# Kernel tuning notes

Measured on AMD Instinct MI355X. Metric: run time of the kernel, lower is better.

The kernel has to match this reference:

```python
import jax, jax.numpy as jnp
import numpy as np

B, N, ENC = 128, 196, 2048
DEC, ATT, EMB, V, T = 512, 512, 512, 10000, 21


def setup_inputs() -> dict:
    key = jax.random.key(0)
    ks = jax.random.split(key, 20)
    g = lambda k, shape, scale=0.02: jax.random.normal(k, shape, dtype=jnp.float32) * scale
    return {
        "features": jax.random.normal(ks[0], (B, N, ENC), dtype=jnp.float32),
        "captions": jax.random.randint(ks[1], (B, T), 0, V),
        "emb": g(ks[2], (V, EMB)),
        # attention (weights stored [in, out])
        "U_w": g(ks[3], (ENC, ATT)), "U_b": jnp.zeros((ATT,), jnp.float32),
        "W_w": g(ks[4], (DEC, ATT)), "W_b": jnp.zeros((ATT,), jnp.float32),
        "A_w": g(ks[5], (ATT, 1)),   "A_b": jnp.zeros((1,), jnp.float32),
        # init hidden state
        "ih_w": g(ks[6], (ENC, DEC)), "ih_b": jnp.zeros((DEC,), jnp.float32),
        "ic_w": g(ks[7], (ENC, DEC)), "ic_b": jnp.zeros((DEC,), jnp.float32),
        # LSTMCell, torch gate order (i, f, g, o); stored [in, 4*DEC]
        "lstm_Wih": g(ks[8], (EMB + ENC, 4 * DEC)),
        "lstm_Whh": g(ks[9], (DEC, 4 * DEC)),
        "lstm_bih": jnp.zeros((4 * DEC,), jnp.float32),
        "lstm_bhh": jnp.zeros((4 * DEC,), jnp.float32),
        # output projection
        "fcn_w": g(ks[10], (DEC, V)), "fcn_b": jnp.zeros((V,), jnp.float32),
    }


def reference(features, captions, emb, U_w, U_b, W_w, W_b, A_w, A_b,
              ih_w, ih_b, ic_w, ic_b,
              lstm_Wih, lstm_Whh, lstm_bih, lstm_bhh, fcn_w, fcn_b):
    # init hidden state from mean-pooled features
    mean_feat = features.mean(axis=1)                      # [B, ENC]
    h0 = mean_feat @ ih_w + ih_b                           # [B, DEC]
    c0 = mean_feat @ ic_w + ic_b

    # U(features) is constant across timesteps -> precompute
    u_hs = jnp.einsum('bne,ea->bna', features, U_w) + U_b  # [B, N, ATT]

    embeds = emb[captions[:, :T - 1]]                       # [B, S, EMB]
    embeds_t = jnp.swapaxes(embeds, 0, 1)                   # [S, B, EMB]

    def step(carry, emb_t):
        h, c = carry
        # Bahdanau attention
        w_ah = h @ W_w + W_b                                # [B, ATT]
        scores = (jnp.tanh(u_hs + w_ah[:, None, :]) @ A_w)[..., 0] + A_b[0]  # [B, N]
        alpha = jax.nn.softmax(scores, axis=1)
        context = jnp.einsum('bn,bne->be', alpha, features) # [B, ENC]
        # LSTMCell
        x = jnp.concatenate([emb_t, context], axis=1)       # [B, EMB+ENC]
        gates = x @ lstm_Wih + lstm_bih + h @ lstm_Whh + lstm_bhh
        i, f, g, o = jnp.split(gates, 4, axis=1)
        c = jax.nn.sigmoid(f) * c + jax.nn.sigmoid(i) * jnp.tanh(g)
        h = jax.nn.sigmoid(o) * jnp.tanh(c)
        out = h @ fcn_w + fcn_b                             # [B, V] (dropout = identity in eval)
        return (h, c), (out, alpha)

    (_, _), (preds_t, alphas_t) = jax.lax.scan(step, (h0, c0), embeds_t)
    preds = jnp.swapaxes(preds_t, 0, 1)                     # [B, S, V]
    alphas = jnp.swapaxes(alphas_t, 0, 1)                   # [B, S, N]
    return preds, alphas
```

## Files before the change

kernel.cpp:

```cpp
#include <hip/hip_runtime.h>
#include <cmath>

#define B_   128
#define N_   196
#define ENC_ 2048
#define DEC_ 512
#define ATT_ 512
#define EMB_ 512
#define V_   10000
#define TS_  20
#define HCAT_ 12672
#define HOUT_ 2560

typedef unsigned short u16;
typedef short s16x8 __attribute__((ext_vector_type(8)));
typedef float f32x4 __attribute__((ext_vector_type(4)));
typedef unsigned short u16x4 __attribute__((ext_vector_type(4)));

__device__ __forceinline__ float sigmoidf_(float x) { return 1.0f / (1.0f + expf(-x)); }

__device__ __forceinline__ u16 f2bf(float x) {
  union { float f; unsigned u; } v; v.f = x;
  unsigned r = v.u + 0x7fff + ((v.u >> 16) & 1);
  return (u16)(r >> 16);
}
__device__ __forceinline__ float bf2f(u16 h) {
  union { float f; unsigned u; } v; v.u = ((unsigned)h) << 16; return v.f;
}

typedef const __attribute__((address_space(1))) void gas_t;
typedef __attribute__((address_space(3))) void las_t;
__device__ __forceinline__ void gld_lds16(const void* g, void* l) {
  __builtin_amdgcn_global_load_lds((gas_t*)g, (las_t*)l, 16, 0, 0);
}

__global__ __launch_bounds__(256, 2) void k_mfma(
    const u16* __restrict__ A, int lda,
    const u16* __restrict__ Bt, int ldb,
    const float* __restrict__ bias,
    float* __restrict__ C, u16* __restrict__ Cb, int ldc, int Nbound,
    float* __restrict__ C2, int csplit, int ldc2,
    int K, int atomic) {
  __shared__ __align__(16) u16 As[128 * 32];
  __shared__ __align__(16) u16 Bs[128 * 32];

  const int tid = threadIdx.x;
  const int bm = blockIdx.y * 128;
  const int bn = blockIdx.x * 128;
  const int kchunk = K / gridDim.z;
  const int k0 = blockIdx.z * kchunk;
  const int kend = k0 + kchunk;

  const int r0 = tid >> 2;
  const int kb = (tid & 3) * 8;
  const u16* ga0 = A + (size_t)(bm + r0) * lda + kb;
  const u16* ga1 = A + (size_t)(bm + 64 + r0) * lda + kb;
  const u16* gb0 = Bt + (size_t)(bn + r0) * ldb + kb;
  const u16* gb1 = Bt + (size_t)(bn + 64 + r0) * ldb + kb;
  u16* la0 = As + tid * 8;
  u16* la1 = As + 2048 + tid * 8;
  u16* lb0 = Bs + tid * 8;
  u16* lb1 = Bs + 2048 + tid * 8;

  const int w = tid >> 6;
  const int lane = tid & 63;
  const int wm = (w & 1) * 64;
  const int wn = (w >> 1) * 64;
  const int r16 = lane & 15;
  const int kq = lane >> 4;

  f32x4 acc[4][4] = {};

  for (int k = k0; k < kend; k += 32) {
    gld_lds16(ga0 + k, la0);
    gld_lds16(ga1 + k, la1);
    gld_lds16(gb0 + k, lb0);
    gld_lds16(gb1 + k, lb1);
    __syncthreads();
    s16x8 af[4], bfr[4];
#pragma unroll
    for (int i = 0; i < 4; ++i)
      af[i] = *(const s16x8*)&As[(wm + i * 16 + r16) * 32 + kq * 8];
#pragma unroll
    for (int i = 0; i < 4; ++i)
      bfr[i] = *(const s16x8*)&Bs[(wn + i * 16 + r16) * 32 + kq * 8];
#pragma unroll
    for (int mi = 0; mi < 4; ++mi)
#pragma unroll
      for (int ni = 0; ni < 4; ++ni)
        acc[mi][ni] = __builtin_amdgcn_mfma_f32_16x16x32_bf16(af[mi], bfr[ni], acc[mi][ni], 0, 0, 0);
    __syncthreads();
  }

#pragma unroll
  for (int ni = 0; ni < 4; ++ni) {
    int col = bn + wn + ni * 16 + r16;
    if (col < Nbound) {
      float bv = bias ? bias[col] : 0.f;
#pragma unroll
      for (int mi = 0; mi < 4; ++mi) {
#pragma unroll
        for (int r = 0; r < 4; ++r) {
          int row = bm + wm + mi * 16 + kq * 4 + r;
          float v = acc[mi][ni][r] + bv;
          if (atomic)                     atomicAdd(&C[(size_t)row * ldc + col], v);
          else if (Cb)                    Cb[(size_t)row * ldc + col] = f2bf(v);
          else if (C2 && col >= csplit)   C2[(size_t)row * ldc2 + (col - csplit)] = v;
          else                            C[(size_t)row * ldc + col] = v;
        }
      }
    }
  }
}

__global__ __launch_bounds__(256) void k_wt(const float* __restrict__ in, int K, int N,
                                            u16* __restrict__ out, int ldo, int Nout) {
  __shared__ float s[32][33];
  int k0 = blockIdx.x * 32, n0 = blockIdx.y * 32;
  int tx = threadIdx.x & 31, ty = threadIdx.x >> 5;
#pragma unroll
  for (int i = 0; i < 4; ++i) {
    int k = k0 + ty + i * 8, n = n0 + tx;
    s[ty + i * 8][tx] = (n < N) ? in[(size_t)k * N + n] : 0.f;
  }
  __syncthreads();
#pragma unroll
  for (int i = 0; i < 4; ++i) {
    int n = n0 + ty + i * 8;
    if (n < Nout) out[(size_t)n * ldo + k0 + tx] = f2bf(s[tx][ty + i * 8]);
  }
}

__global__ __launch_bounds__(256) void k_hbias(const float* __restrict__ W_b,
                                               const float* __restrict__ bih,
                                               const float* __restrict__ bhh,
                                               const float* __restrict__ fcn_b,
                                               float* __restrict__ hbias) {
  int i = blockIdx.x * 256 + threadIdx.x;
  if (i >= HCAT_) return;
  float v;
  if (i < 512)        v = W_b[i];
  else if (i < 2560)  v = bih[i - 512] + bhh[i - 512];
  else if (i < 12560) v = fcn_b[i - 2560];
  else                v = 0.f;
  hbias[i] = v;
}

__global__ __launch_bounds__(256) void k_embed_all(const float* __restrict__ emb,
                                                   const int* __restrict__ captions,
                                                   u16* __restrict__ emb_all_bf) {
  int r = blockIdx.y;
  int t = r >> 7, b = r & 127;
  int k = blockIdx.x * 256 + threadIdx.x;
  int tok = captions[b * 21 + t];
  emb_all_bf[(size_t)r * EMB_ + k] = f2bf(emb[(size_t)tok * EMB_ + k]);
}

__global__ __launch_bounds__(256) void k_cvtmean(const float* __restrict__ f,
                                                 u16* __restrict__ feat_bf,
                                                 u16* __restrict__ mean_bf) {
  int b = blockIdx.y;
  int e = blockIdx.x * 256 + threadIdx.x;
  const float* p = f + (size_t)b * N_ * ENC_ + e;
  u16* q = feat_bf + (size_t)b * N_ * ENC_ + e;
  float s = 0.f;
#pragma unroll 4
  for (int n = 0; n < N_; ++n) {
    float v = p[(size_t)n * ENC_];
    s += v;
    q[(size_t)n * ENC_] = f2bf(v);
  }
  mean_bf[b * ENC_ + e] = f2bf(s * (1.0f / (float)N_));
}

__global__ __launch_bounds__(256) void k_scores(const u16* __restrict__ u_hs,
                                                const float* __restrict__ w_ah, int ldw,
                                                const float* __restrict__ A_w,
                                                const float* __restrict__ A_b,
                                                float* __restrict__ scores) {
  int wave = threadIdx.x >> 6;
  int lane = threadIdx.x & 63;
  int bn = blockIdx.x * 4 + wave;
  int b = bn / N_;
  int a0 = lane * 8;
  const u16* up = u_hs + (size_t)bn * ATT_ + a0;
  const float* wp = w_ah + (size_t)b * ldw + a0;
  float s = 0.f;
#pragma unroll
  for (int j = 0; j < 2; ++j) {
    u16x4 uv = *(const u16x4*)(up + j * 4);
    float4 wv = *(const float4*)(wp + j * 4);
    float4 aw = *(const float4*)(A_w + a0 + j * 4);
    s += tanhf(bf2f(uv.x) + wv.x) * aw.x;
    s += tanhf(bf2f(uv.y) + wv.y) * aw.y;
    s += tanhf(bf2f(uv.z) + wv.z) * aw.z;
    s += tanhf(bf2f(uv.w) + wv.w) * aw.w;
  }
#pragma unroll
  for (int off = 32; off; off >>= 1) s += __shfl_down(s, off);
  if (lane == 0) scores[bn] = s + A_b[0];
}

__global__ __launch_bounds__(256) void k_ctx(const float* __restrict__ scores,
                                             const u16* __restrict__ feat_bf,
                                             const float* __restrict__ embg_t,
                                             const float* __restrict__ houtt,
                                             float* __restrict__ gates,
                                             float* __restrict__ alphas, int t,
                                             u16* __restrict__ ctx_bf) {
  int b = blockIdx.y, tid = threadIdx.x;
  int w = tid >> 6, lane = tid & 63;

  {
    int j0 = blockIdx.x * 1024 + tid * 4;
    float4 eg = *(const float4*)(embg_t + (size_t)b * 2048 + j0);
    float4 hg = *(const float4*)(houtt + (size_t)b * HOUT_ + 512 + j0);
    float4 o; o.x = eg.x + hg.x; o.y = eg.y + hg.y; o.z = eg.z + hg.z; o.w = eg.w + hg.w;
    *(float4*)(gates + (size_t)b * 2048 + j0) = o;
  }

  __shared__ float al[N_];
  __shared__ float wm[4], ws[4];
  __shared__ float bmax, bsum;
  float v = (tid < N_) ? scores[b * N_ + tid] : -1e30f;
  float m = v;
#pragma unroll
  for (int off = 32; off; off >>= 1) m = fmaxf(m, __shfl_down(m, off));
  if (lane == 0) wm[w] = m;
  __syncthreads();
  if (tid == 0) bmax = fmaxf(fmaxf(wm[0], wm[1]), fmaxf(wm[2], wm[3]));
  __syncthreads();
  float e = (tid < N_) ? expf(v - bmax) : 0.f;
  float s = e;
#pragma unroll
  for (int off = 32; off; off >>= 1) s += __shfl_down(s, off);
  if (lane == 0) ws[w] = s;
  __syncthreads();
  if (tid == 0) bsum = ws[0] + ws[1] + ws[2] + ws[3];
  __syncthreads();
  float a = e / bsum;
  if (tid < N_) {
    al[tid] = a;
    if (blockIdx.x == 0) alphas[((size_t)b * TS_ + t) * N_ + tid] = a;
  }
  __syncthreads();

  int e0 = blockIdx.x * 1024 + tid * 4;
  const u16* fp = feat_bf + (size_t)b * N_ * ENC_ + e0;
  float s0 = 0, s1 = 0, s2 = 0, s3 = 0;
#pragma unroll 4
  for (int n = 0; n < N_; ++n) {
    u16x4 vv = *(const u16x4*)(fp + (size_t)n * ENC_);
    float av = al[n];
    s0 += av * bf2f(vv.x); s1 += av * bf2f(vv.y);
    s2 += av * bf2f(vv.z); s3 += av * bf2f(vv.w);
  }
  u16x4 o; o.x = f2bf(s0); o.y = f2bf(s1); o.z = f2bf(s2); o.w = f2bf(s3);
  *(u16x4*)(ctx_bf + (size_t)b * ENC_ + e0) = o;
}

__global__ __launch_bounds__(256) void k_lstm(const float* __restrict__ gates,
                                              float* __restrict__ c,
                                              u16* __restrict__ h_bf) {
  int b = blockIdx.y;
  int j = blockIdx.x * 256 + threadIdx.x;
  const float* g = gates + (size_t)b * 2048;
  float ig = sigmoidf_(g[j]);
  float fg = sigmoidf_(g[512 + j]);
  float gg = tanhf(g[1024 + j]);
  float og = sigmoidf_(g[1536 + j]);
  float cn = fg * c[b * DEC_ + j] + ig * gg;
  c[b * DEC_ + j] = cn;
  h_bf[(size_t)b * DEC_ + j] = f2bf(og * tanhf(cn));
}

extern "C" void kernel_launch(void* const* d_in, const int* in_sizes, int n_in,
                              void* d_out, int out_size, void* d_ws, size_t ws_size,
                              hipStream_t stream) {
  (void)in_sizes; (void)n_in; (void)out_size; (void)ws_size;

  const float* features = (const float*)d_in[0];
  const int*   captions = (const int*)d_in[1];
  const float* emb      = (const float*)d_in[2];
  const float* U_w      = (const float*)d_in[3];
  const float* U_b      = (const float*)d_in[4];
  const float* W_w      = (const float*)d_in[5];
  const float* W_b      = (const float*)d_in[6];
  const float* A_w      = (const float*)d_in[7];
  const float* A_b      = (const float*)d_in[8];
  const float* ih_w     = (const float*)d_in[9];
  const float* ih_b     = (const float*)d_in[10];
  const float* ic_w     = (const float*)d_in[11];
  const float* ic_b     = (const float*)d_in[12];
  const float* Wih      = (const float*)d_in[13];
  const float* Whh      = (const float*)d_in[14];
  const float* bih      = (const float*)d_in[15];
  const float* bhh      = (const float*)d_in[16];
  const float* fcn_w    = (const float*)d_in[17];
  const float* fcn_b    = (const float*)d_in[18];

  float* preds  = (float*)d_out;
  float* alphas = (float*)d_out + (size_t)B_ * TS_ * V_;

  float* p = (float*)d_ws;
  u16*   u_hs      = (u16*)p;    p += (size_t)B_ * N_ * ATT_ / 2;
  u16*   feat_bf   = (u16*)p;    p += (size_t)B_ * N_ * ENC_ / 2;
  u16*   hcatT     = (u16*)p;    p += (size_t)HCAT_ * DEC_ / 2;
  u16*   U_wT      = (u16*)p;    p += (size_t)ATT_ * ENC_ / 2;
  u16*   ih_wT     = (u16*)p;    p += (size_t)DEC_ * ENC_ / 2;
  u16*   ic_wT     = (u16*)p;    p += (size_t)DEC_ * ENC_ / 2;
  u16*   WihEmbT   = (u16*)p;    p += (size_t)2048 * EMB_ / 2;
  u16*   WihCtxT   = (u16*)p;    p += (size_t)2048 * ENC_ / 2;
  u16*   mean_bf   = (u16*)p;    p += (size_t)B_ * ENC_ / 2;
  u16*   emb_all   = (u16*)p;    p += (size_t)TS_ * B_ * EMB_ / 2;
  u16*   h_bf      = (u16*)p;    p += (size_t)B_ * DEC_ / 2;
  u16*   ctx_bf    = (u16*)p;    p += (size_t)B_ * ENC_ / 2;
  float* embgates  = p;          p += (size_t)TS_ * B_ * 2048;
  float* houtt     = p;          p += (size_t)B_ * HOUT_;
  float* cbuf      = p;          p += (size_t)B_ * DEC_;
  float* scores    = p;          p += (size_t)B_ * N_;
  float* gates     = p;          p += (size_t)B_ * 2048;
  float* hbias     = p;          p += HCAT_;

  k_cvtmean<<<dim3(ENC_ / 256, B_), 256, 0, stream>>>(features, feat_bf, mean_bf);
  k_wt<<<dim3(ENC_ / 32, ATT_ / 32), 256, 0, stream>>>(U_w, ENC_, ATT_, U_wT, ENC_, ATT_);
  k_wt<<<dim3(ENC_ / 32, DEC_ / 32), 256, 0, stream>>>(ih_w, ENC_, DEC_, ih_wT, ENC_, DEC_);
  k_wt<<<dim3(ENC_ / 32, DEC_ / 32), 256, 0, stream>>>(ic_w, ENC_, DEC_, ic_wT, ENC_, DEC_);
  k_wt<<<dim3(DEC_ / 32, ATT_ / 32), 256, 0, stream>>>(W_w, DEC_, ATT_, hcatT, DEC_, ATT_);
  k_wt<<<dim3(DEC_ / 32, 2048 / 32), 256, 0, stream>>>(Whh, DEC_, 2048, hcatT + (size_t)512 * DEC_, DEC_, 2048);
  k_wt<<<dim3(DEC_ / 32, 10112 / 32), 256, 0, stream>>>(fcn_w, DEC_, V_, hcatT + (size_t)2560 * DEC_, DEC_, 10112);
  k_wt<<<dim3(EMB_ / 32, 2048 / 32), 256, 0, stream>>>(Wih, EMB_, 2048, WihEmbT, EMB_, 2048);
  k_wt<<<dim3(ENC_ / 32, 2048 / 32), 256, 0, stream>>>(Wih + (size_t)EMB_ * 2048, ENC_, 2048, WihCtxT, ENC_, 2048);
  k_hbias<<<(HCAT_ + 255) / 256, 256, 0, stream>>>(W_b, bih, bhh, fcn_b, hbias);
  k_embed_all<<<dim3(EMB_ / 256, TS_ * B_), 256, 0, stream>>>(emb, captions, emb_all);

  k_mfma<<<dim3(4, 1, 1), 256, 0, stream>>>(mean_bf, ENC_, ih_wT, ENC_, ih_b,
                                            nullptr, h_bf, DEC_, DEC_, nullptr, 0, 0, ENC_, 0);
  k_mfma<<<dim3(4, 1, 1), 256, 0, stream>>>(mean_bf, ENC_, ic_wT, ENC_, ic_b,
                                            cbuf, nullptr, DEC_, DEC_, nullptr, 0, 0, ENC_, 0);
  k_mfma<<<dim3(ATT_ / 128, (B_ * N_) / 128, 1), 256, 0, stream>>>(
      feat_bf, ENC_, U_wT, ENC_, U_b, nullptr, u_hs, ATT_, ATT_, nullptr, 0, 0, ENC_, 0);
  k_mfma<<<dim3(2048 / 128, TS_, 1), 256, 0, stream>>>(
      emb_all, EMB_, WihEmbT, EMB_, nullptr, embgates, nullptr, 2048, 2048, nullptr, 0, 0, EMB_, 0);

  for (int t = 0; t < TS_; ++t) {
    if (t == 0) {
      k_mfma<<<dim3(HOUT_ / 128, 1, 1), 256, 0, stream>>>(
          h_bf, DEC_, hcatT, DEC_, hbias, houtt, nullptr, HOUT_, HOUT_,
          nullptr, 0, 0, DEC_, 0);
    } else {
      k_mfma<<<dim3(HCAT_ / 128, 1, 1), 256, 0, stream>>>(
          h_bf, DEC_, hcatT, DEC_, hbias, houtt, nullptr, HOUT_, 12560,
          preds + (size_t)(t - 1) * V_, HOUT_, TS_ * V_, DEC_, 0);
    }

    k_scores<<<(B_ * N_) / 4, 256, 0, stream>>>(u_hs, houtt, HOUT_, A_w, A_b, scores);

    k_ctx<<<dim3(2, B_), 256, 0, stream>>>(scores, feat_bf, embgates + (size_t)t * B_ * 2048,
                                           houtt, gates, alphas, t, ctx_bf);

    k_mfma<<<dim3(2048 / 128, 1, 8), 256, 0, stream>>>(
        ctx_bf, ENC_, WihCtxT, ENC_, nullptr, gates, nullptr, 2048, 2048, nullptr, 0, 0, ENC_, 1);

    k_lstm<<<dim3(DEC_ / 256, B_), 256, 0, stream>>>(gates, cbuf, h_bf);
  }

  k_mfma<<<dim3(10112 / 128, 1, 1), 256, 0, stream>>>(
      h_bf, DEC_, hcatT + (size_t)2560 * DEC_, DEC_, hbias + 2560,
      preds + (size_t)(TS_ - 1) * V_, nullptr, TS_ * V_, V_, nullptr, 0, 0, DEC_, 0);
}
```

Baseline: 1.956 ms.

## Double-buffer GEMM LDS tiles, vectorize feature conversion, use fast tanh in scores

The MFMA GEMM now uses two LDS buffers and issues the global-to-LDS loads for the next K tile before computing the current one, removing one barrier per iteration so memory latency can overlap with MFMA work. The feature conversion/mean kernel processes four floats per thread with vector loads and stores, using a quarter as many blocks. The attention score kernel replaces tanhf with an exp/rcp-based approximation clamped at ±8. Double buffering doubles LDS per block, which may limit occupancy, and the fast tanh slightly changes numerics.

```diff
diff --git a/kernel.cpp b/kernel.cpp
--- a/kernel.cpp
+++ b/kernel.cpp
@@ -19,6 +19,12 @@
 
 __device__ __forceinline__ float sigmoidf_(float x) { return 1.0f / (1.0f + expf(-x)); }
 
+__device__ __forceinline__ float fast_tanh(float x) {
+  float cx = fminf(fmaxf(x, -8.f), 8.f);
+  float e = __expf(2.f * cx);
+  return (e - 1.f) * __builtin_amdgcn_rcpf(e + 1.f);
+}
+
 __device__ __forceinline__ u16 f2bf(float x) {
   union { float f; unsigned u; } v; v.f = x;
   unsigned r = v.u + 0x7fff + ((v.u >> 16) & 1);
@@ -41,8 +47,8 @@
     float* __restrict__ C, u16* __restrict__ Cb, int ldc, int Nbound,
     float* __restrict__ C2, int csplit, int ldc2,
     int K, int atomic) {
-  __shared__ __align__(16) u16 As[128 * 32];
-  __shared__ __align__(16) u16 Bs[128 * 32];
+  __shared__ __align__(16) u16 As[2][128 * 32];
+  __shared__ __align__(16) u16 Bs[2][128 * 32];
 
   const int tid = threadIdx.x;
   const int bm = blockIdx.y * 128;
@@ -57,10 +63,6 @@
   const u16* ga1 = A + (size_t)(bm + 64 + r0) * lda + kb;
   const u16* gb0 = Bt + (size_t)(bn + r0) * ldb + kb;
   const u16* gb1 = Bt + (size_t)(bn + 64 + r0) * ldb + kb;
-  u16* la0 = As + tid * 8;
-  u16* la1 = As + 2048 + tid * 8;
-  u16* lb0 = Bs + tid * 8;
-  u16* lb1 = Bs + 2048 + tid * 8;
 
   const int w = tid >> 6;
   const int lane = tid & 63;
@@ -71,25 +73,32 @@
 
   f32x4 acc[4][4] = {};
 
+  auto STAGE = [&](int buf, int k) {
+    gld_lds16(ga0 + k, &As[buf][tid * 8]);
+    gld_lds16(ga1 + k, &As[buf][2048 + tid * 8]);
+    gld_lds16(gb0 + k, &Bs[buf][tid * 8]);
+    gld_lds16(gb1 + k, &Bs[buf][2048 + tid * 8]);
+  };
+
+  STAGE(0, k0);
+  __syncthreads();
+  int cur = 0;
   for (int k = k0; k < kend; k += 32) {
-    gld_lds16(ga0 + k, la0);
-    gld_lds16(ga1 + k, la1);
-    gld_lds16(gb0 + k, lb0);
-    gld_lds16(gb1 + k, lb1);
-    __syncthreads();
+    if (k + 32 < kend) STAGE(cur ^ 1, k + 32);
     s16x8 af[4], bfr[4];
 #pragma unroll
     for (int i = 0; i < 4; ++i)
-      af[i] = *(const s16x8*)&As[(wm + i * 16 + r16) * 32 + kq * 8];
+      af[i] = *(const s16x8*)&As[cur][(wm + i * 16 + r16) * 32 + kq * 8];
 #pragma unroll
     for (int i = 0; i < 4; ++i)
-      bfr[i] = *(const s16x8*)&Bs[(wn + i * 16 + r16) * 32 + kq * 8];
+      bfr[i] = *(const s16x8*)&Bs[cur][(wn + i * 16 + r16) * 32 + kq * 8];
 #pragma unroll
     for (int mi = 0; mi < 4; ++mi)
 #pragma unroll
       for (int ni = 0; ni < 4; ++ni)
         acc[mi][ni] = __builtin_amdgcn_mfma_f32_16x16x32_bf16(af[mi], bfr[ni], acc[mi][ni], 0, 0, 0);
     __syncthreads();
+    cur ^= 1;
   }
 
 #pragma unroll
@@ -160,17 +169,21 @@
                                                  u16* __restrict__ feat_bf,
                                                  u16* __restrict__ mean_bf) {
   int b = blockIdx.y;
-  int e = blockIdx.x * 256 + threadIdx.x;
+  int e = (blockIdx.x * 256 + threadIdx.x) * 4;
   const float* p = f + (size_t)b * N_ * ENC_ + e;
   u16* q = feat_bf + (size_t)b * N_ * ENC_ + e;
-  float s = 0.f;
-#pragma unroll 4
+  float s0 = 0.f, s1 = 0.f, s2 = 0.f, s3 = 0.f;
+#pragma unroll 2
   for (int n = 0; n < N_; ++n) {
-    float v = p[(size_t)n * ENC_];
-    s += v;
-    q[(size_t)n * ENC_] = f2bf(v);
-  }
-  mean_bf[b * ENC_ + e] = f2bf(s * (1.0f / (float)N_));
+    float4 v = *(const float4*)(p + (size_t)n * ENC_);
+    s0 += v.x; s1 += v.y; s2 += v.z; s3 += v.w;
+    u16x4 o; o.x = f2bf(v.x); o.y = f2bf(v.y); o.z = f2bf(v.z); o.w = f2bf(v.w);
+    *(u16x4*)(q + (size_t)n * ENC_) = o;
+  }
+  const float inv = 1.0f / (float)N_;
+  u16x4 m; m.x = f2bf(s0 * inv); m.y = f2bf(s1 * inv);
+  m.z = f2bf(s2 * inv); m.w = f2bf(s3 * inv);
+  *(u16x4*)(mean_bf + b * ENC_ + e) = m;
 }
 
 __global__ __launch_bounds__(256) void k_scores(const u16* __restrict__ u_hs,
@@ -191,10 +204,10 @@
     u16x4 uv = *(const u16x4*)(up + j * 4);
     float4 wv = *(const float4*)(wp + j * 4);
     float4 aw = *(const float4*)(A_w + a0 + j * 4);
-    s += tanhf(bf2f(uv.x) + wv.x) * aw.x;
-    s += tanhf(bf2f(uv.y) + wv.y) * aw.y;
-    s += tanhf(bf2f(uv.z) + wv.z) * aw.z;
-    s += tanhf(bf2f(uv.w) + wv.w) * aw.w;
+    s += fast_tanh(bf2f(uv.x) + wv.x) * aw.x;
+    s += fast_tanh(bf2f(uv.y) + wv.y) * aw.y;
+    s += fast_tanh(bf2f(uv.z) + wv.z) * aw.z;
+    s += fast_tanh(bf2f(uv.w) + wv.w) * aw.w;
   }
 #pragma unroll
   for (int off = 32; off; off >>= 1) s += __shfl_down(s, off);
@@ -322,7 +335,7 @@
   float* gates     = p;          p += (size_t)B_ * 2048;
   float* hbias     = p;          p += HCAT_;
 
-  k_cvtmean<<<dim3(ENC_ / 256, B_), 256, 0, stream>>>(features, feat_bf, mean_bf);
+  k_cvtmean<<<dim3(ENC_ / 1024, B_), 256, 0, stream>>>(features, feat_bf, mean_bf);
   k_wt<<<dim3(ENC_ / 32, ATT_ / 32), 256, 0, stream>>>(U_w, ENC_, ATT_, U_wT, ENC_, ATT_);
   k_wt<<<dim3(ENC_ / 32, DEC_ / 32), 256, 0, stream>>>(ih_w, ENC_, DEC_, ih_wT, ENC_, DEC_);
   k_wt<<<dim3(ENC_ / 32, DEC_ / 32), 256, 0, stream>>>(ic_w, ENC_, DEC_, ic_wT, ENC_, DEC_);
```

Result: faster. 1.885 ms (-3.6%).
